# Kernel tuning notes

Measured on AMD Instinct MI355X. Metric: run time of the kernel, lower is better.

## Reference

```python
import jax, jax.numpy as jnp
import numpy as np

C = 256  # inplanes == planes
EPS = 1e-5


def _cb(p):
    # per-channel param -> broadcastable NCHW
    return p[None, :, None, None]


def binary_act(x):
    # forward: sign(x); backward: piecewise-polynomial STE
    poly = jnp.where(x < -1.0, -1.0,
           jnp.where(x < 0.0, x * x + 2.0 * x,
           jnp.where(x < 1.0, -x * x + 2.0 * x, 1.0)))
    return jax.lax.stop_gradient(jnp.sign(x) - poly) + poly


def bin_weight(w):
    # forward: per-out-channel mean(|w|) * sign(w); backward: through clamp(w,-1,1)
    scale = jax.lax.stop_gradient(jnp.mean(jnp.abs(w), axis=(1, 2, 3), keepdims=True))
    cl = jnp.clip(w, -1.0, 1.0)
    return jax.lax.stop_gradient(scale * jnp.sign(w) - cl) + cl


def conv(x, w, pad):
    return jax.lax.conv_general_dilated(
        x, w, window_strides=(1, 1), padding=((pad, pad), (pad, pad)),
        dimension_numbers=('NCHW', 'OIHW', 'NCHW'))


def bn(x, g, b, m, v):
    inv = g * jax.lax.rsqrt(v + EPS)
    return x * _cb(inv) + _cb(b - m * inv)


def prelu(x, a):
    return jnp.where(x > 0, x, _cb(a) * x)


def setup_inputs() -> dict:
    key = jax.random.key(0)
    ks = jax.random.split(key, 3)
    z = jnp.zeros((C,), jnp.float32)
    o = jnp.ones((C,), jnp.float32)
    return {
        'x':  jax.random.normal(ks[0], (32, C, 56, 56), jnp.float32),
        'w3': jax.random.uniform(ks[1], (C, C, 3, 3), jnp.float32) * 0.001,
        'w1': jax.random.uniform(ks[2], (C, C, 1, 1), jnp.float32) * 0.001,
        'b11': z, 'b12': z, 'b13': z, 'b21': z, 'b22': z, 'b23': z,
        'g1': o, 'be1': z, 'm1': z, 'v1': o,
        'g2': o, 'be2': z, 'm2': z, 'v2': o,
        'a1': jnp.full((C,), 0.25, jnp.float32),
        'a2': jnp.full((C,), 0.25, jnp.float32),
    }


def reference(x, w3, w1, b11, b12, b13, b21, b22, b23,
              g1, be1, m1, v1, g2, be2, m2, v2, a1, a2):
    # branch 1: bias -> binarize -> binary 3x3 conv -> BN -> residual
    out1 = binary_act(x + _cb(b11))
    out1 = conv(out1, bin_weight(w3), pad=1)
    out1 = bn(out1, g1, be1, m1, v1)
    out1 = x + out1
    out1 = prelu(out1 + _cb(b12), a1) + _cb(b13)
    # branch 2: bias -> binarize -> binary 1x1 conv -> BN -> residual
    out2 = binary_act(out1 + _cb(b21))
    out2 = conv(out2, bin_weight(w1), pad=0)
    out2 = bn(out2, g2, be2, m2, v2) + out1
    out2 = prelu(out2 + _cb(b22), a2) + _cb(b23)
    return out2
```

## Files before the change

### kernel.cpp

```cpp
#include <hip/hip_runtime.h>
#include <hip/hip_bf16.h>


#define CCH  256
#define PIMG 3136
#define SPIX 3364
#define WPAD 58

typedef __attribute__((ext_vector_type(4))) int intx4;

#define GLOAD16(gp, lp) __builtin_amdgcn_global_load_lds( \
    (const __attribute__((address_space(1))) unsigned int*)(gp), \
    (__attribute__((address_space(3))) unsigned int*)(lp), 16, 0, 0)

__device__ __forceinline__ signed char sgnc(float v) {
    return (v > 0.f) ? 1 : ((v < 0.f) ? -1 : 0);
}

__global__ void transpose_sign(const float* __restrict__ x,
                               const float* __restrict__ b11,
                               signed char* __restrict__ spad) {
    const int hp  = blockIdx.x;
    const int cbg = blockIdx.y;
    const int n   = blockIdx.z;
    const int t   = threadIdx.x;
    __shared__ __align__(16) signed char tile[128 * 60];

    const bool border_h = (hp == 0) || (hp == 57);
    if (!border_h) {
        const int h = hp - 1;
        for (int it = 0; it < 7; ++it) {
            int lin  = t + it * 256;
            int c    = lin / 14;
            int col4 = lin - c * 14;
            int cg   = cbg * 128 + c;
            const float4 xv = *(const float4*)(x +
                ((size_t)(n * CCH + cg)) * PIMG + h * 56 + col4 * 4);
            float bb = b11[cg];
            int w = (sgnc(xv.x + bb) & 0xff)
                  | ((sgnc(xv.y + bb) & 0xff) << 8)
                  | ((sgnc(xv.z + bb) & 0xff) << 16)
                  | ((sgnc(xv.w + bb) & 0xff) << 24);
            *(int*)(&tile[c * 60 + col4 * 4]) = w;
        }
    }
    __syncthreads();
    for (int it = 0; it < 8; ++it) {
        int lin = t + it * 256;
        if (lin >= 58 * 32) break;
        int wp = lin >> 5;
        int c  = (lin & 31) * 4;
        int w  = 0;
        if (!border_h && wp >= 1 && wp <= 56) {
            signed char s0 = tile[(c + 0) * 60 + (wp - 1)];
            signed char s1 = tile[(c + 1) * 60 + (wp - 1)];
            signed char s2 = tile[(c + 2) * 60 + (wp - 1)];
            signed char s3 = tile[(c + 3) * 60 + (wp - 1)];
            w = (s0 & 0xff) | ((s1 & 0xff) << 8) | ((s2 & 0xff) << 16) | ((s3 & 0xff) << 24);
        }
        *(int*)(spad + (((size_t)cbg * 32 + n) * SPIX + hp * WPAD + wp) * 128 + c) = w;
    }
}

__global__ void prep_w(const float* __restrict__ w3, const float* __restrict__ w1,
                       const float* __restrict__ g1, const float* __restrict__ be1,
                       const float* __restrict__ m1, const float* __restrict__ v1,
                       const float* __restrict__ g2, const float* __restrict__ be2,
                       const float* __restrict__ m2, const float* __restrict__ v2,
                       signed char* __restrict__ wq3f, signed char* __restrict__ wq1f,
                       float* __restrict__ k2s, float* __restrict__ k2b,
                       float* __restrict__ k3s, float* __restrict__ k3b) {
    const int o = blockIdx.x;
    const int t = threadIdx.x;
    __shared__ float red[256];
    if (o < 256) {
        const float* wp = w3 + (size_t)o * 2304;
        float s = 0.f;
        for (int i = t; i < 2304; i += 256) s += fabsf(wp[i]);
        red[t] = s; __syncthreads();
        for (int k = 128; k > 0; k >>= 1) { if (t < k) red[t] += red[t + k]; __syncthreads(); }
        float scale = red[0] * (1.0f / 2304.0f);
        for (int i = t; i < 2304; i += 256) {
            int c = i / 9; int r9 = i - c * 9;
            int cbg = c >> 7, cl = c & 127;
            int ks = cl >> 6, qd = (cl >> 4) & 3, b = cl & 15;
            wq3f[(size_t)(((r9 * 2 + cbg) * 2 + ks)) * 16384 +
                 (o >> 4) * 1024 + qd * 256 + (o & 15) * 16 + b] = sgnc(wp[i]);
        }
        if (t == 0) {
            float inv = g1[o] * rsqrtf(v1[o] + 1e-5f);
            k2s[o] = scale * inv;
            k2b[o] = be1[o] - m1[o] * inv;
        }
    } else {
        const int o1 = o - 256;
        float w = w1[(size_t)o1 * 256 + t];
        red[t] = fabsf(w); __syncthreads();
        for (int k = 128; k > 0; k >>= 1) { if (t < k) red[t] += red[t + k]; __syncthreads(); }
        float scale = red[0] * (1.0f / 256.0f);
        int cbg = t >> 7, cl = t & 127;
        int ks = cl >> 6, qd = (cl >> 4) & 3, b = cl & 15;
        wq1f[(size_t)((cbg * 2 + ks)) * 16384 +
             (o1 >> 4) * 1024 + qd * 256 + (o1 & 15) * 16 + b] = sgnc(w);
        if (t == 0) {
            float inv = g2[o1] * rsqrtf(v2[o1] + 1e-5f);
            k3s[o1] = scale * inv;
            k3b[o1] = be2[o1] - m2[o1] * inv;
        }
    }
}


#define LOADP(ph, af, bf) { \
    const int cbg_ = (ph) / 18, rem_ = (ph) % 18, r9_ = rem_ >> 1, ks_ = rem_ & 1; \
    const int shift_ = (r9_ / 3) * WPAD + (r9_ % 3); \
    const signed char* bp_ = wq3f + \
        (size_t)((((r9_ * 2 + cbg_) * 2 + ks_) * 16 + wid * 4) * 1024) + lane * 16; \
    _Pragma("unroll") \
    for (int j_ = 0; j_ < 4; ++j_) bf[j_] = *(const intx4*)(bp_ + j_ * 1024); \
    _Pragma("unroll") \
    for (int i_ = 0; i_ < 4; ++i_) { \
        const int r_  = prow[i_] + shift_; \
        const int gg_ = (ks_ * 4 + quad) ^ (r_ & 7); \
        af[i_] = *(const intx4*)(&As[cbg_][r_ * 128 + gg_ * 16]); \
    } }

#define MFMAP(af, bf) { \
    __builtin_amdgcn_s_setprio(1); \
    _Pragma("unroll") \
    for (int i_ = 0; i_ < 4; ++i_) \
        _Pragma("unroll") \
        for (int j_ = 0; j_ < 4; ++j_) \
            acc[i_][j_] = __builtin_amdgcn_mfma_i32_16x16x64_i8( \
                af[i_], bf[j_], acc[i_][j_], 0, 0, 0); \
    __builtin_amdgcn_s_setprio(0); }

__global__ __launch_bounds__(256, 2) void gemm_fused(
    const signed char* __restrict__ spad, const signed char* __restrict__ wq3f,
    const signed char* __restrict__ wq1f, const float* __restrict__ x,
    const float* __restrict__ k2s, const float* __restrict__ k2b,
    const float* __restrict__ k3s, const float* __restrict__ k3b,
    const float* __restrict__ b12, const float* __restrict__ b13,
    const float* __restrict__ b21, const float* __restrict__ a1,
    const float* __restrict__ b22, const float* __restrict__ b23,
    const float* __restrict__ a2, float* __restrict__ out) {
    __shared__ __align__(16) signed char As[2][192 * 128];
    const int t    = threadIdx.x;
    const int tile = blockIdx.x;
    const int n    = blockIdx.y;
    const int lane = t & 63;
    const int wid  = t >> 6;
    const int quad = lane >> 4;
    const int l16  = lane & 15;

    const int p0t    = tile * 64;
    const int h0     = p0t / 56;
    const int w0     = p0t - h0 * 56;
    const int pstart = h0 * WPAD + w0;

    int prow[4];
    #pragma unroll
    for (int i = 0; i < 4; ++i) {
        int p = p0t + i * 16 + l16;
        int h = p / 56, w = p - h * 56;
        prow[i] = h * WPAD + w - pstart;
    }

    const int rbase = wid * 8 + (lane >> 3);
    const int gsw   = (lane & 7) ^ (rbase & 7);

    for (int cbg = 0; cbg < 2; ++cbg) {
        const size_t cbase = ((size_t)(cbg * 32 + n)) * SPIX + pstart;
        #pragma unroll
        for (int k = 0; k < 6; ++k) {
            const int row = k * 32 + rbase;
            const signed char* gp = spad + (cbase + row) * 128 + gsw * 16;
            GLOAD16(gp, &As[cbg][(k * 4 + wid) * 1024]);
        }
    }
    __syncthreads();

    intx4 acc[4][4] = {};
    {
        intx4 afA[4], bfA[4], afB[4], bfB[4];
        LOADP(0, afA, bfA)
        #pragma unroll
        for (int ph = 0; ph < 36; ph += 2) {
            if (ph + 1 < 36) LOADP(ph + 1, afB, bfB)
            MFMAP(afA, bfA)
            if (ph + 2 < 36) LOADP(ph + 2, afA, bfA)
            if (ph + 1 < 36) MFMAP(afB, bfB)
        }
    }

    __syncthreads();

    signed char* sgnL = &As[0][0];

    float out1r[4][4][4];
    #pragma unroll
    for (int j = 0; j < 4; ++j) {
        const int o = wid * 64 + j * 16 + l16;
        const float sc = k2s[o], bt = k2b[o];
        const float v12 = b12[o], v13 = b13[o], v21 = b21[o], va = a1[o];
        #pragma unroll
        for (int i = 0; i < 4; ++i) {
            const int p0 = p0t + i * 16 + quad * 4;
            const float4 xv = *(const float4*)(x + ((size_t)(n * CCH + o)) * PIMG + p0);
            float rr[4] = {xv.x, xv.y, xv.z, xv.w};
            #pragma unroll
            for (int r = 0; r < 4; ++r) {
                float v  = (float)acc[i][j][r] * sc + bt + rr[r];
                float tt = v + v12;
                float o1 = ((tt > 0.f) ? tt : va * tt) + v13;
                out1r[i][j][r] = o1;
                const int pl = i * 16 + quad * 4 + r;
                sgnL[pl * 256 + (((wid * 4 + j) ^ (pl & 15)) << 4) + l16] =
                    sgnc(o1 + v21);
            }
        }
    }
    __syncthreads();

    intx4 acc2[4][4] = {};
    #pragma unroll
    for (int ph = 0; ph < 4; ++ph) {
        const int cbg2 = ph >> 1, ks2 = ph & 1;
        intx4 af2[4], bf2[4];
        const signed char* bp = wq1f +
            (size_t)(((cbg2 * 2 + ks2) * 16 + wid * 4) * 1024) + lane * 16;
        #pragma unroll
        for (int j = 0; j < 4; ++j) bf2[j] = *(const intx4*)(bp + j * 1024);
        const int q16 = cbg2 * 8 + ks2 * 4 + quad;
        #pragma unroll
        for (int i = 0; i < 4; ++i) {
            const int m = i * 16 + l16;
            af2[i] = *(const intx4*)(&sgnL[m * 256 + ((q16 ^ (m & 15)) << 4)]);
        }
        #pragma unroll
        for (int i = 0; i < 4; ++i)
            #pragma unroll
            for (int j = 0; j < 4; ++j)
                acc2[i][j] = __builtin_amdgcn_mfma_i32_16x16x64_i8(
                    af2[i], bf2[j], acc2[i][j], 0, 0, 0);
    }

    #pragma unroll
    for (int j = 0; j < 4; ++j) {
        const int o = wid * 64 + j * 16 + l16;
        const float sc = k3s[o], bt = k3b[o];
        const float v22 = b22[o], v23 = b23[o], va = a2[o];
        #pragma unroll
        for (int i = 0; i < 4; ++i) {
            const int p0 = p0t + i * 16 + quad * 4;
            float res[4];
            #pragma unroll
            for (int r = 0; r < 4; ++r) {
                float v  = (float)acc2[i][j][r] * sc + bt + out1r[i][j][r];
                float tt = v + v22;
                res[r] = ((tt > 0.f) ? tt : va * tt) + v23;
            }
            float4 ov; ov.x = res[0]; ov.y = res[1]; ov.z = res[2]; ov.w = res[3];
            *(float4*)(out + ((size_t)(n * CCH + o)) * PIMG + p0) = ov;
        }
    }
}

extern "C" void kernel_launch(void* const* d_in, const int* in_sizes, int n_in,
                              void* d_out, int out_size, void* d_ws, size_t ws_size,
                              hipStream_t stream) {
    const float* x   = (const float*)d_in[0];
    const float* w3  = (const float*)d_in[1];
    const float* w1  = (const float*)d_in[2];
    const float* b11 = (const float*)d_in[3];
    const float* b12 = (const float*)d_in[4];
    const float* b13 = (const float*)d_in[5];
    const float* b21 = (const float*)d_in[6];
    const float* b22 = (const float*)d_in[7];
    const float* b23 = (const float*)d_in[8];
    const float* g1  = (const float*)d_in[9];
    const float* be1 = (const float*)d_in[10];
    const float* m1  = (const float*)d_in[11];
    const float* v1  = (const float*)d_in[12];
    const float* g2  = (const float*)d_in[13];
    const float* be2 = (const float*)d_in[14];
    const float* m2  = (const float*)d_in[15];
    const float* v2  = (const float*)d_in[16];
    const float* a1  = (const float*)d_in[17];
    const float* a2  = (const float*)d_in[18];
    float* out = (float*)d_out;

    char* ws = (char*)d_ws;
    signed char* spad = (signed char*)(ws);
    signed char* wq3f = (signed char*)(ws + 27816192);
    signed char* wq1f = (signed char*)(ws + 28406016);
    float* k2s = (float*)(ws + 28471552);
    float* k2b = k2s + 256;
    float* k3s = k2s + 512;
    float* k3b = k2s + 768;

    transpose_sign<<<dim3(58, 2, 32), 256, 0, stream>>>(x, b11, spad);
    prep_w<<<512, 256, 0, stream>>>(w3, w1, g1, be1, m1, v1, g2, be2, m2, v2,
                                    wq3f, wq1f, k2s, k2b, k3s, k3b);
    gemm_fused<<<dim3(49, 32), 256, 0, stream>>>(spad, wq3f, wq1f, x,
                                                 k2s, k2b, k3s, k3b,
                                                 b12, b13, b21, a1,
                                                 b22, b23, a2, out);
}
```

Baseline: 304.8 us.

## Deepen weight prefetch pipeline in GEMM and vectorize sign-transpose with byte perms

The main GEMM loop now splits A (LDS) and B (global weight) fragment loads. B fragments are prefetched three phases ahead in a 4-deep register ring, while A stays double-buffered, so global weight load latency is better hidden behind MFMAs. The transpose_sign kernel now writes border rows as zeros and returns early, and builds the interior transpose with 32-bit LDS reads and v_perm byte shuffles instead of single-byte gathers. The deeper ring raises register pressure, which could hurt occupancy at the two-waves bound.

```diff
diff --git a/kernel.cpp b/kernel.cpp
--- a/kernel.cpp
+++ b/kernel.cpp
@@ -26,39 +26,64 @@
     const int t   = threadIdx.x;
     __shared__ __align__(16) signed char tile[128 * 60];
 
-    const bool border_h = (hp == 0) || (hp == 57);
-    if (!border_h) {
-        const int h = hp - 1;
-        for (int it = 0; it < 7; ++it) {
-            int lin  = t + it * 256;
-            int c    = lin / 14;
-            int col4 = lin - c * 14;
-            int cg   = cbg * 128 + c;
-            const float4 xv = *(const float4*)(x +
-                ((size_t)(n * CCH + cg)) * PIMG + h * 56 + col4 * 4);
-            float bb = b11[cg];
-            int w = (sgnc(xv.x + bb) & 0xff)
-                  | ((sgnc(xv.y + bb) & 0xff) << 8)
-                  | ((sgnc(xv.z + bb) & 0xff) << 16)
-                  | ((sgnc(xv.w + bb) & 0xff) << 24);
-            *(int*)(&tile[c * 60 + col4 * 4]) = w;
-        }
+    const size_t obase = ((size_t)cbg * 32 + n) * SPIX + (size_t)hp * WPAD;
+
+    if (hp == 0 || hp == 57) {
+        for (int it = 0; it < 8; ++it) {
+            int lin = t + it * 256;
+            if (lin >= 1856) break;
+            int wp = lin >> 5;
+            int c4 = (lin & 31) * 4;
+            *(int*)(spad + (obase + wp) * 128 + c4) = 0;
+        }
+        return;
+    }
+
+    const int h = hp - 1;
+    for (int it = 0; it < 7; ++it) {
+        int lin  = t + it * 256;
+        int c    = lin / 14;
+        int col4 = lin - c * 14;
+        int cg   = cbg * 128 + c;
+        const float4 xv = *(const float4*)(x +
+            ((size_t)(n * CCH + cg)) * PIMG + h * 56 + col4 * 4);
+        float bb = b11[cg];
+        int w = (sgnc(xv.x + bb) & 0xff)
+              | ((sgnc(xv.y + bb) & 0xff) << 8)
+              | ((sgnc(xv.z + bb) & 0xff) << 16)
+              | ((sgnc(xv.w + bb) & 0xff) << 24);
+        *(int*)(&tile[c * 60 + col4 * 4]) = w;
     }
     __syncthreads();
-    for (int it = 0; it < 8; ++it) {
-        int lin = t + it * 256;
-        if (lin >= 58 * 32) break;
-        int wp = lin >> 5;
-        int c  = (lin & 31) * 4;
-        int w  = 0;
-        if (!border_h && wp >= 1 && wp <= 56) {
-            signed char s0 = tile[(c + 0) * 60 + (wp - 1)];
-            signed char s1 = tile[(c + 1) * 60 + (wp - 1)];
-            signed char s2 = tile[(c + 2) * 60 + (wp - 1)];
-            signed char s3 = tile[(c + 3) * 60 + (wp - 1)];
-            w = (s0 & 0xff) | ((s1 & 0xff) << 8) | ((s2 & 0xff) << 16) | ((s3 & 0xff) << 24);
-        }
-        *(int*)(spad + (((size_t)cbg * 32 + n) * SPIX + hp * WPAD + wp) * 128 + c) = w;
+
+    for (int it = 0; it < 2; ++it) {
+        int task = t + it * 256;
+        if (task >= 480) break;
+        int g  = task >> 5;
+        int c4 = task & 31;
+        unsigned int w[4];
+        #pragma unroll
+        for (int cc = 0; cc < 4; ++cc) {
+            const signed char* rowp = &tile[(c4 * 4 + cc) * 60];
+            unsigned int A = (g == 0)  ? 0u : *(const unsigned int*)(rowp + (g - 1) * 4);
+            unsigned int B = (g < 14)  ? *(const unsigned int*)(rowp + g * 4) : 0u;
+            w[cc] = (A >> 24) | (B << 8);
+        }
+        unsigned int p01_0 = __builtin_amdgcn_perm(w[1], w[0], 0x05010400u);
+        unsigned int p01_1 = __builtin_amdgcn_perm(w[1], w[0], 0x07030602u);
+        unsigned int p23_0 = __builtin_amdgcn_perm(w[3], w[2], 0x05010400u);
+        unsigned int p23_1 = __builtin_amdgcn_perm(w[3], w[2], 0x07030602u);
+        unsigned int o0 = __builtin_amdgcn_perm(p23_0, p01_0, 0x05040100u);
+        unsigned int o1 = __builtin_amdgcn_perm(p23_0, p01_0, 0x07060302u);
+        unsigned int o2 = __builtin_amdgcn_perm(p23_1, p01_1, 0x05040100u);
+        unsigned int o3 = __builtin_amdgcn_perm(p23_1, p01_1, 0x07060302u);
+        unsigned int ov[4] = {o0, o1, o2, o3};
+        #pragma unroll
+        for (int p = 0; p < 4; ++p) {
+            int wp = 4 * g + p;
+            if (wp < 58)
+                *(int*)(spad + (obase + wp) * 128 + c4 * 4) = (int)ov[p];
+        }
     }
 }
 
@@ -111,13 +136,16 @@
 }
 
 
-#define LOADP(ph, af, bf) { \
+#define LOADB(ph, bf) { \
     const int cbg_ = (ph) / 18, rem_ = (ph) % 18, r9_ = rem_ >> 1, ks_ = rem_ & 1; \
-    const int shift_ = (r9_ / 3) * WPAD + (r9_ % 3); \
     const signed char* bp_ = wq3f + \
         (size_t)((((r9_ * 2 + cbg_) * 2 + ks_) * 16 + wid * 4) * 1024) + lane * 16; \
     _Pragma("unroll") \
-    for (int j_ = 0; j_ < 4; ++j_) bf[j_] = *(const intx4*)(bp_ + j_ * 1024); \
+    for (int j_ = 0; j_ < 4; ++j_) bf[j_] = *(const intx4*)(bp_ + j_ * 1024); }
+
+#define LOADA(ph, af) { \
+    const int cbg_ = (ph) / 18, rem_ = (ph) % 18, r9_ = rem_ >> 1, ks_ = rem_ & 1; \
+    const int shift_ = (r9_ / 3) * WPAD + (r9_ % 3); \
     _Pragma("unroll") \
     for (int i_ = 0; i_ < 4; ++i_) { \
         const int r_  = prow[i_] + shift_; \
@@ -182,14 +210,16 @@
 
     intx4 acc[4][4] = {};
     {
-        intx4 afA[4], bfA[4], afB[4], bfB[4];
-        LOADP(0, afA, bfA)
-        #pragma unroll
-        for (int ph = 0; ph < 36; ph += 2) {
-            if (ph + 1 < 36) LOADP(ph + 1, afB, bfB)
-            MFMAP(afA, bfA)
-            if (ph + 2 < 36) LOADP(ph + 2, afA, bfA)
-            if (ph + 1 < 36) MFMAP(afB, bfB)
+        intx4 bfS[4][4], afS[2][4];
+        LOADB(0, bfS[0])
+        LOADB(1, bfS[1])
+        LOADB(2, bfS[2])
+        LOADA(0, afS[0])
+        #pragma unroll
+        for (int ph = 0; ph < 36; ++ph) {
+            if (ph + 1 < 36) LOADA(ph + 1, afS[(ph + 1) & 1])
+            if (ph + 3 < 36) LOADB(ph + 3, bfS[(ph + 3) & 3])
+            MFMAP(afS[ph & 1], bfS[ph & 3])
         }
     }
 
```

Result: no change. 302.6 us (-0.7%).
